# Optimization experiments

Measured on AMD Instinct MI355X. Metric: run time of the kernel, lower is better.

The kernel has to match this reference:

```python
import jax, jax.numpy as jnp
import numpy as np
from jax import lax

B, C, H, W = 8, 384, 32, 32
HEADS, GROUPS = 12, 3
CG = C // GROUPS          # 128 channels per offset group
HD = C // HEADS           # 32 head dim
NS = H * W                # sampled kv points (one per query location)
EPS = 1e-5


def setup_inputs() -> dict:
    key = jax.random.key(0)
    ks = jax.random.split(key, 10)
    w = lambda k, sh, sc=0.02: (jax.random.normal(k, sh, jnp.float32) * sc)
    return {
        "x1": jax.random.normal(ks[0], (B, C, H, W), jnp.float32),
        "x2": jax.random.normal(ks[1], (B, C, H, W), jnp.float32),
        "Wq": w(ks[2], (C, C)), "bq": jnp.zeros((C,), jnp.float32),
        "Wk": w(ks[3], (C, C)), "bk": jnp.zeros((C,), jnp.float32),
        "Wv": w(ks[4], (C, C)), "bv": jnp.zeros((C,), jnp.float32),
        "Wo": w(ks[5], (C, C)), "bo": jnp.zeros((C,), jnp.float32),
        "off_dw": w(ks[6], (CG, 1, 5, 5)),       # depthwise 5x5 offset conv
        "off_dw_b": jnp.zeros((CG,), jnp.float32),
        "ln_g": jnp.ones((CG,), jnp.float32),
        "ln_b": jnp.zeros((CG,), jnp.float32),
        "off_w": w(ks[7], (2, CG), 0.01),         # 1x1 conv -> 2 offset channels
    }


def _conv1x1(x, Wm, bm):
    return jnp.einsum('oc,bchw->bohw', Wm, x) + bm[None, :, None, None]


def _ref_grid():
    # normalized reference points in [-1,1], channel 0 = x (width), 1 = y (height)
    xs = (jnp.arange(W, dtype=jnp.float32) + 0.5) / W * 2.0 - 1.0
    ys = (jnp.arange(H, dtype=jnp.float32) + 0.5) / H * 2.0 - 1.0
    gy, gx = jnp.meshgrid(ys, xs, indexing='ij')   # [H,W]
    return jnp.stack([gx, gy], axis=0)             # [2,H,W]


def _forward(x1, x2, Wq, bq, Wk, bk, Wv, bv, Wo, bo,
             off_dw, off_dw_b, ln_g, ln_b, off_w):
    BG = B * GROUPS
    q = _conv1x1(x1, Wq, bq)                                   # [B,C,H,W]

    # --- offset network (per group) ---
    qg = q.reshape(BG, CG, H, W)
    t = lax.conv_general_dilated(qg, off_dw, (1, 1), 'SAME',
                                 dimension_numbers=('NCHW', 'OIHW', 'NCHW'),
                                 feature_group_count=CG)
    t = t + off_dw_b[None, :, None, None]
    mu = jnp.mean(t, axis=1, keepdims=True)
    var = jnp.var(t, axis=1, keepdims=True)
    t = (t - mu) * lax.rsqrt(var + EPS)
    t = t * ln_g[None, :, None, None] + ln_b[None, :, None, None]
    t = jax.nn.gelu(t)
    off = jnp.einsum('oc,bchw->bohw', off_w, t)                # [BG,2,H,W]

    pos = jnp.clip(off + _ref_grid()[None], -1.0, 1.0)         # [BG,2,H,W]
    px = pos[:, 0].reshape(BG, NS)
    py = pos[:, 1].reshape(BG, NS)

    # --- bilinear grid_sample of x2 (align_corners=True) ---
    ix = (px + 1.0) * 0.5 * (W - 1)
    iy = (py + 1.0) * 0.5 * (H - 1)
    x0f, y0f = jnp.floor(ix), jnp.floor(iy)
    wx, wy = ix - x0f, iy - y0f
    x0 = jnp.clip(x0f.astype(jnp.int32), 0, W - 1)
    x1i = jnp.clip(x0 + 1, 0, W - 1)
    y0 = jnp.clip(y0f.astype(jnp.int32), 0, H - 1)
    y1i = jnp.clip(y0 + 1, 0, H - 1)

    x2g = x2.reshape(BG, CG, H * W)

    def gather(yi, xi):
        idx = yi * W + xi                                      # [BG,NS]
        idx = jnp.broadcast_to(idx[:, None, :], (BG, CG, NS))
        return jnp.take_along_axis(x2g, idx, axis=2)           # [BG,CG,NS]

    v00, v01 = gather(y0, x0), gather(y0, x1i)
    v10, v11 = gather(y1i, x0), gather(y1i, x1i)
    wx_, wy_ = wx[:, None, :], wy[:, None, :]
    samp = (v00 * (1 - wx_) * (1 - wy_) + v01 * wx_ * (1 - wy_)
            + v10 * (1 - wx_) * wy_ + v11 * wx_ * wy_)         # [BG,CG,NS]
    samp = samp.reshape(B, C, NS)

    # --- multi-head attention between q and sampled k/v ---
    k = jnp.einsum('oc,bcn->bon', Wk, samp) + bk[None, :, None]
    v = jnp.einsum('oc,bcn->bon', Wv, samp) + bv[None, :, None]
    qf = q.reshape(B, HEADS, HD, NS)
    kf = k.reshape(B, HEADS, HD, NS)
    vf = v.reshape(B, HEADS, HD, NS)
    scale = 1.0 / np.sqrt(HD).astype(np.float32)
    attn = jax.nn.softmax(jnp.einsum('bhdq,bhdk->bhqk', qf * scale, kf), axis=-1)
    out = jnp.einsum('bhqk,bhdk->bhdq', attn, vf).reshape(B, C, H, W)
    y = _conv1x1(out, Wo, bo)
    return x1 + y                                              # residual add (drop_path=0 -> Identity)


def reference(x1, x2, Wq, bq, Wk, bk, Wv, bv, Wo, bo,
              off_dw, off_dw_b, ln_g, ln_b, off_w):
    return _forward(x1, x2, Wq, bq, Wk, bk, Wv, bv, Wo, bo,
                    off_dw, off_dw_b, ln_g, ln_b, off_w)
```

## Files before the change

### kernel.cpp

```cpp
#include <hip/hip_runtime.h>
#include <math.h>

#define B_  8
#define C_  384
#define NS_ 1024
#define HEADS_ 12
#define HD_ 32
#define GROUPS_ 3
#define CG_ 128
#define EPS_ 1e-5f
#define QSC2 (0.17677669529663687f * 1.4426950408889634f)

typedef __attribute__((ext_vector_type(8))) short bf16x8;
typedef __attribute__((ext_vector_type(4))) short bf16x4;
typedef __attribute__((ext_vector_type(4))) float f32x4;
typedef __attribute__((ext_vector_type(8))) __bf16 b8;

static __device__ __forceinline__ short f2b(float f) {
  union { float f; unsigned u; } v; v.f = f;
  unsigned r = v.u + 0x7fffu + ((v.u >> 16) & 1u);
  return (short)(r >> 16);
}
static __device__ __forceinline__ float b2f(short s) {
  union { unsigned u; float f; } v; v.u = ((unsigned)(unsigned short)s) << 16;
  return v.f;
}

#if __has_builtin(__builtin_amdgcn_exp2f)
#define EXP2(x) __builtin_amdgcn_exp2f(x)
#else
#define EXP2(x) exp2f(x)
#endif

static __device__ __forceinline__ unsigned cvtpk(float lo, float hi) {
  unsigned r;
  asm("v_cvt_pk_bf16_f32 %0, %1, %2" : "=v"(r) : "v"(lo), "v"(hi));
  return r;
}

static __device__ __forceinline__ f32x4 MFMA(bf16x8 a, bf16x8 b, f32x4 c) {
  return __builtin_amdgcn_mfma_f32_16x16x32_bf16(
      __builtin_bit_cast(b8, a), __builtin_bit_cast(b8, b), c, 0, 0, 0);
}

__global__ __launch_bounds__(256) void prep(
    const float* __restrict__ x1, const float* __restrict__ x2,
    const float* __restrict__ Wq, const float* __restrict__ Wk,
    const float* __restrict__ Wv, const float* __restrict__ Wo,
    const float* __restrict__ dw,
    short* __restrict__ x1t, short* __restrict__ x2t,
    short* __restrict__ Wqb, short* __restrict__ Wkb,
    short* __restrict__ Wvb, short* __restrict__ Wob,
    float* __restrict__ dwp) {
  __shared__ float tl[32][33];
  int id = blockIdx.x;
  int tid = threadIdx.x;
  int tx = tid & 31, ty = tid >> 5;
  if (id < 3072) {
    int nb = id & 31, cb = (id >> 5) % 12, b = id / 384;
    int n0 = nb * 32, c0 = cb * 32;
#pragma unroll
    for (int i = 0; i < 4; ++i)
      tl[ty + 8 * i][tx] = x1[((size_t)b * C_ + c0 + ty + 8 * i) * NS_ + n0 + tx];
    __syncthreads();
#pragma unroll
    for (int i = 0; i < 4; ++i)
      x1t[((size_t)b * NS_ + n0 + ty + 8 * i) * C_ + c0 + tx] = f2b(tl[tx][ty + 8 * i]);
  } else if (id < 6144) {
    int i = id - 3072;
    int nb = i & 31, cb = (i >> 5) & 3, bg = i / 128;
    int n0 = nb * 32, c0 = cb * 32;
#pragma unroll
    for (int j = 0; j < 4; ++j)
      tl[ty + 8 * j][tx] = x2[((size_t)bg * CG_ + c0 + ty + 8 * j) * NS_ + n0 + tx];
    __syncthreads();
#pragma unroll
    for (int j = 0; j < 4; ++j)
      x2t[((size_t)bg * NS_ + n0 + ty + 8 * j) * CG_ + c0 + tx] = f2b(tl[tx][ty + 8 * j]);
  } else if (id < 8448) {
    int i = id - 6144;
    int mat = i / 576;
    int e = (i % 576) * 256 + tid;
    const float* s = mat == 0 ? Wq : mat == 1 ? Wk : mat == 2 ? Wv : Wo;
    short*       d = mat == 0 ? Wqb : mat == 1 ? Wkb : mat == 2 ? Wvb : Wob;
    d[e] = f2b(s[e]);
  } else {
    int e = (id - 8448) * 256 + tid;
    if (e < 25 * CG_) { int t = e / CG_, c = e % CG_; dwp[e] = dw[c * 25 + t]; }
  }
}

#define GLOADA(kc_, AF)                                                        \
  _Pragma("unroll")                                                            \
  for (int rt = 0; rt < 4; ++rt)                                               \
    AF[rt] = *(const bf16x8*)(Ab + (size_t)(n0 + wr + rt * 16 + r15) * C_ +    \
                              (kc_) + g * 8);
#define GLOADB(kc_, BF, WP, MOFF)                                              \
  _Pragma("unroll")                                                            \
  for (int ct = 0; ct < 4; ++ct)                                               \
    BF[ct] = *(const bf16x8*)((WP) + (size_t)((MOFF) + ct * 16 + r15) * C_ +   \
                              (kc_) + g * 8);
#define GMFMA(AF, BF)                                                          \
  _Pragma("unroll")                                                            \
  for (int rt = 0; rt < 4; ++rt)                                               \
    _Pragma("unroll")                                                          \
    for (int ct = 0; ct < 4; ++ct) acc[rt][ct] = MFMA(AF[rt], BF[ct], acc[rt][ct]);

template <int MODE>
__global__ __launch_bounds__(256) void gemm_nm(
    const short* __restrict__ A, const short* __restrict__ Wb,
    const float* __restrict__ bias, const float* __restrict__ res,
    short* __restrict__ outb, float* __restrict__ outf) {
  int b = blockIdx.z;
  int n0 = blockIdx.x * 128;
  int m0 = blockIdx.y * 128;
  int wv = threadIdx.x >> 6;
  int lane = threadIdx.x & 63;
  int g = lane >> 4, r15 = lane & 15;
  int wr = (wv >> 1) * 64, wc = (wv & 1) * 64;

  const short* Ab = A + (size_t)b * NS_ * C_;
  f32x4 acc[4][4];
#pragma unroll
  for (int i = 0; i < 4; ++i)
#pragma unroll
    for (int j = 0; j < 4; ++j) acc[i][j] = (f32x4){0.f, 0.f, 0.f, 0.f};

  bf16x8 afA[4], bfA[4], afB[4], bfB[4];
  GLOADA(0, afA); GLOADB(0, bfA, Wb, m0 + wc);
#pragma unroll
  for (int cp = 0; cp < 6; ++cp) {
    GLOADA(64 * cp + 32, afB); GLOADB(64 * cp + 32, bfB, Wb, m0 + wc);
    GMFMA(afA, bfA);
    if (cp < 5) { GLOADA(64 * cp + 64, afA); GLOADB(64 * cp + 64, bfA, Wb, m0 + wc); }
    GMFMA(afB, bfB);
  }

#pragma unroll
  for (int rt = 0; rt < 4; ++rt)
#pragma unroll
    for (int ct = 0; ct < 4; ++ct) {
      int m = m0 + wc + ct * 16 + r15;
      int nb = n0 + wr + rt * 16 + g * 4;
      float bv = bias[m];
      f32x4 v = acc[rt][ct];
      v.x += bv; v.y += bv; v.z += bv; v.w += bv;
      if (MODE == 1) {
        *(f32x4*)(outf + ((size_t)b * C_ + m) * NS_ + nb) = v;
        outb[((size_t)b * NS_ + nb + 0) * C_ + m] = f2b(v.x * QSC2);
        outb[((size_t)b * NS_ + nb + 1) * C_ + m] = f2b(v.y * QSC2);
        outb[((size_t)b * NS_ + nb + 2) * C_ + m] = f2b(v.z * QSC2);
        outb[((size_t)b * NS_ + nb + 3) * C_ + m] = f2b(v.w * QSC2);
      } else {
        const f32x4 rv = *(const f32x4*)(res + ((size_t)b * C_ + m) * NS_ + nb);
        v.x += rv.x; v.y += rv.y; v.z += rv.z; v.w += rv.w;
        *(f32x4*)(outf + ((size_t)b * C_ + m) * NS_ + nb) = v;
      }
    }
}

__global__ __launch_bounds__(256) void gemm_kv(
    const short* __restrict__ A, const short* __restrict__ Wkb,
    const short* __restrict__ Wvb, const float* __restrict__ bkv,
    const float* __restrict__ bvv, short* __restrict__ kblk,
    short* __restrict__ vblk) {
  int b = blockIdx.z;
  int n0 = blockIdx.x * 128;
  int m0 = blockIdx.y * 64;
  int wv = threadIdx.x >> 6;
  int lane = threadIdx.x & 63;
  int g = lane >> 4, r15 = lane & 15;
  int wr = (wv >> 1) * 64;
  int isv = wv & 1;
  const short* Wsel = isv ? Wvb : Wkb;
  const float* bsel = isv ? bvv : bkv;

  const short* Ab = A + (size_t)b * NS_ * C_;
  f32x4 acc[4][4];
#pragma unroll
  for (int i = 0; i < 4; ++i)
#pragma unroll
    for (int j = 0; j < 4; ++j) acc[i][j] = (f32x4){0.f, 0.f, 0.f, 0.f};

  bf16x8 afA[4], bfA[4], afB[4], bfB[4];
  GLOADA(0, afA); GLOADB(0, bfA, Wsel, m0);
#pragma unroll
  for (int cp = 0; cp < 6; ++cp) {
    GLOADA(64 * cp + 32, afB); GLOADB(64 * cp + 32, bfB, Wsel, m0);
    GMFMA(afA, bfA);
    if (cp < 5) { GLOADA(64 * cp + 64, afA); GLOADB(64 * cp + 64, bfA, Wsel, m0); }
    GMFMA(afB, bfB);
  }

#pragma unroll
  for (int rt = 0; rt < 4; ++rt)
#pragma unroll
    for (int ct = 0; ct < 4; ++ct) {
      int m = m0 + ct * 16 + r15;
      int nb = n0 + wr + rt * 16 + g * 4;
      float bv = bsel[m];
      f32x4 v = acc[rt][ct];
      v.x += bv; v.y += bv; v.z += bv; v.w += bv;
      int h = m >> 5, dh = m & 31;
      if (!isv) {
        size_t hb = ((size_t)(b * HEADS_ + h) * 32 + (nb >> 5)) * 1024 +
                    (((nb >> 4) & 1) ? 512 : 0);
        int base_l = (nb & 15) | ((dh >> 3) << 4);
        int jj = dh & 7;
        kblk[hb + (size_t)(base_l + 0) * 8 + jj] = f2b(v.x);
        kblk[hb + (size_t)(base_l + 1) * 8 + jj] = f2b(v.y);
        kblk[hb + (size_t)(base_l + 2) * 8 + jj] = f2b(v.z);
        kblk[hb + (size_t)(base_l + 3) * 8 + jj] = f2b(v.w);
      } else {
        int dt = dh >> 4, q15v = dh & 15;
        int kk = nb & 31;
        int half = kk >> 4, gk = (kk & 15) >> 2;
        size_t off = ((size_t)(b * HEADS_ + h) * 32 + (nb >> 5)) * 1024 +
                     dt * 512 + (size_t)((q15v | (gk << 4))) * 8 + half * 4;
        bf16x4 s4 = {f2b(v.x), f2b(v.y), f2b(v.z), f2b(v.w)};
        *(bf16x4*)(vblk + off) = s4;
      }
    }
}

__global__ __launch_bounds__(256) void offsample4(
    const float* __restrict__ qd, const short* __restrict__ x2t,
    const float* __restrict__ dwp, const float* __restrict__ dwb,
    const float* __restrict__ lng, const float* __restrict__ lnb,
    const float* __restrict__ offw, short* __restrict__ samp) {
  int bg = blockIdx.x, y = blockIdx.y;
  int tid = threadIdx.x;
  int xg = tid >> 5, cc = tid & 31;
  int x0 = xg << 2, c0 = cc << 2;

  const float* qb = qd + ((size_t)bg * CG_ + c0) * NS_;

  f32x4 dwb4 = *(const f32x4*)(dwb + c0);
  float a[4][4];
#pragma unroll
  for (int i = 0; i < 4; ++i)
#pragma unroll
    for (int p = 0; p < 4; ++p) a[i][p] = dwb4[i];

#pragma unroll
  for (int dy = -2; dy <= 2; ++dy) {
    int yy = y + dy;
    if (yy < 0 || yy > 31) continue;
    f32x4 w0 = *(const f32x4*)(dwp + ((dy + 2) * 5 + 0) * CG_ + c0);
    f32x4 w1 = *(const f32x4*)(dwp + ((dy + 2) * 5 + 1) * CG_ + c0);
    f32x4 w2 = *(const f32x4*)(dwp + ((dy + 2) * 5 + 2) * CG_ + c0);
    f32x4 w3 = *(const f32x4*)(dwp + ((dy + 2) * 5 + 3) * CG_ + c0);
    f32x4 w4 = *(const f32x4*)(dwp + ((dy + 2) * 5 + 4) * CG_ + c0);
#pragma unroll
    for (int i = 0; i < 4; ++i) {
      const float* row = qb + (size_t)i * NS_ + yy * 32;
      f32x4 wa = (f32x4){0.f, 0.f, 0.f, 0.f};
      f32x4 wcv = (f32x4){0.f, 0.f, 0.f, 0.f};
      if (x0 >= 4)  wa  = *(const f32x4*)(row + x0 - 4);
      f32x4 wb = *(const f32x4*)(row + x0);
      if (x0 <= 24) wcv = *(const f32x4*)(row + x0 + 4);
      float w[12] = {wa[0], wa[1], wa[2], wa[3], wb[0], wb[1], wb[2], wb[3],
                     wcv[0], wcv[1], wcv[2], wcv[3]};
      float wt[5] = {w0[i], w1[i], w2[i], w3[i], w4[i]};
#pragma unroll
      for (int p = 0; p < 4; ++p)
#pragma unroll
        for (int j = 0; j < 5; ++j)
          a[i][p] = fmaf(w[p + j + 2], wt[j], a[i][p]);
    }
  }

  f32x4 sum = (f32x4){0.f, 0.f, 0.f, 0.f}, sumsq = sum;
#pragma unroll
  for (int i = 0; i < 4; ++i)
#pragma unroll
    for (int p = 0; p < 4; ++p) { sum[p] += a[i][p]; sumsq[p] += a[i][p] * a[i][p]; }
#pragma unroll
  for (int m = 1; m <= 16; m <<= 1) {
#pragma unroll
    for (int p = 0; p < 4; ++p) {
      sum[p]   += __shfl_xor(sum[p], m);
      sumsq[p] += __shfl_xor(sumsq[p], m);
    }
  }
  f32x4 mu, rs;
#pragma unroll
  for (int p = 0; p < 4; ++p) {
    mu[p] = sum[p] * (1.f / CG_);
    float var = sumsq[p] * (1.f / CG_) - mu[p] * mu[p];
    rs[p] = rsqrtf(var + EPS_);
  }

  f32x4 lg = *(const f32x4*)(lng + c0);
  f32x4 lb = *(const f32x4*)(lnb + c0);
  f32x4 ow0 = *(const f32x4*)(offw + c0);
  f32x4 ow1 = *(const f32x4*)(offw + CG_ + c0);
  f32x4 o0 = (f32x4){0.f, 0.f, 0.f, 0.f}, o1 = o0;
#pragma unroll
  for (int i = 0; i < 4; ++i)
#pragma unroll
    for (int p = 0; p < 4; ++p) {
      float z = (a[i][p] - mu[p]) * rs[p] * lg[i] + lb[i];
      float u = z * fmaf(0.044715f * z, z, 1.f);
      float e = __expf(-1.5957691216057308f * u);
      float ge = z * __builtin_amdgcn_rcpf(1.f + e);
      o0[p] = fmaf(ow0[i], ge, o0[p]);
      o1[p] = fmaf(ow1[i], ge, o1[p]);
    }
#pragma unroll
  for (int m = 1; m <= 16; m <<= 1) {
#pragma unroll
    for (int p = 0; p < 4; ++p) {
      o0[p] += __shfl_xor(o0[p], m);
      o1[p] += __shfl_xor(o1[p], m);
    }
  }

  int b = bg / GROUPS_, gi = bg % GROUPS_;
  const short* xb = x2t + (size_t)bg * NS_ * CG_ + c0;
  float gy = (y + 0.5f) * 0.0625f - 1.f;
#pragma unroll
  for (int p = 0; p < 4; ++p) {
    int x = x0 + p, n = y * 32 + x;
    float gx = (x + 0.5f) * 0.0625f - 1.f;
    float px = fminf(fmaxf(o0[p] + gx, -1.f), 1.f);
    float py = fminf(fmaxf(o1[p] + gy, -1.f), 1.f);
    float ix = (px + 1.f) * 0.5f * 31.f;
    float iy = (py + 1.f) * 0.5f * 31.f;
    float x0f = floorf(ix), y0f = floorf(iy);
    float wx = ix - x0f, wy = iy - y0f;
    int xa = min(max((int)x0f, 0), 31), xbb = min(xa + 1, 31);
    int ya = min(max((int)y0f, 0), 31), yb = min(ya + 1, 31);
    int i00 = ya * 32 + xa, i01 = ya * 32 + xbb;
    int i10 = yb * 32 + xa, i11 = yb * 32 + xbb;
    float w00 = (1.f - wx) * (1.f - wy), w01 = wx * (1.f - wy);
    float w10 = (1.f - wx) * wy,         w11 = wx * wy;
    bf16x4 v00 = *(const bf16x4*)(xb + (size_t)i00 * CG_);
    bf16x4 v01 = *(const bf16x4*)(xb + (size_t)i01 * CG_);
    bf16x4 v10 = *(const bf16x4*)(xb + (size_t)i10 * CG_);
    bf16x4 v11 = *(const bf16x4*)(xb + (size_t)i11 * CG_);
    short out4[4];
#pragma unroll
    for (int j = 0; j < 4; ++j) {
      float v = w00 * b2f(v00[j]) + w01 * b2f(v01[j]) +
                w10 * b2f(v10[j]) + w11 * b2f(v11[j]);
      out4[j] = f2b(v);
    }
    *(bf16x4*)(samp + ((size_t)b * NS_ + n) * C_ + gi * CG_ + c0) = *(bf16x4*)out4;
  }
}

__global__ __launch_bounds__(256) void attn_split(
    const short* __restrict__ qn, const short* __restrict__ kblk,
    const short* __restrict__ vblk, short* __restrict__ op0,
    short* __restrict__ op1, float* __restrict__ lp) {
  int L = blockIdx.x;
  int tq = L >> 3;
  int task = (L & 7) + ((tq % 24) << 3);
  int qblk = tq / 24;
  int bh = task >> 1, s = task & 1;
  int b = bh / HEADS_, h = bh % HEADS_;
  int wv = threadIdx.x >> 6, lane = threadIdx.x & 63;
  int g = lane >> 4, q15 = lane & 15;
  int q0 = qblk * 128 + wv * 32;

  const short* Qb = qn + (size_t)b * NS_ * C_ + h * HD_;
  const short* Kc = kblk + ((size_t)(b * HEADS_ + h) * 32 + s * 16) * 1024 + lane * 8;
  const short* Vc = vblk + ((size_t)(b * HEADS_ + h) * 32 + s * 16) * 1024 + lane * 8;

  bf16x8 qf[2];
  qf[0] = *(const bf16x8*)(Qb + (size_t)(q0 + q15) * C_ + g * 8);
  qf[1] = *(const bf16x8*)(Qb + (size_t)(q0 + 16 + q15) * C_ + g * 8);

  f32x4 o[2][2];
  o[0][0] = o[0][1] = o[1][0] = o[1][1] = (f32x4){0.f, 0.f, 0.f, 0.f};
  f32x4 lv[2];
  lv[0] = lv[1] = (f32x4){0.f, 0.f, 0.f, 0.f};

#define LOADC(c_, K0, K1, V0, V1)                                              \
  {                                                                            \
    K0 = *(const bf16x8*)(Kc + (c_) * 1024);                                   \
    K1 = *(const bf16x8*)(Kc + (c_) * 1024 + 512);                             \
    V0 = *(const bf16x8*)(Vc + (c_) * 1024);                                   \
    V1 = *(const bf16x8*)(Vc + (c_) * 1024 + 512);                             \
  }

#define COMPUTEC(K0, K1, V0, V1)                                               \
  {                                                                            \
    _Pragma("unroll")                                                          \
    for (int qt = 0; qt < 2; ++qt) {                                           \
      f32x4 z_ = {0.f, 0.f, 0.f, 0.f};                                         \
      f32x4 t0 = MFMA(K0, qf[qt], z_);                                         \
      f32x4 t1 = MFMA(K1, qf[qt], z_);                                         \
      f32x4 e0, e1;                                                            \
      e0.x = EXP2(t0.x); e0.y = EXP2(t0.y); e0.z = EXP2(t0.z); e0.w = EXP2(t0.w);\
      e1.x = EXP2(t1.x); e1.y = EXP2(t1.y); e1.z = EXP2(t1.z); e1.w = EXP2(t1.w);\
      lv[qt] += e0; lv[qt] += e1;                                              \
      union { unsigned u[4]; bf16x8 v; } pu;                                   \
      pu.u[0] = cvtpk(e0.x, e0.y);                                             \
      pu.u[1] = cvtpk(e0.z, e0.w);                                             \
      pu.u[2] = cvtpk(e1.x, e1.y);                                             \
      pu.u[3] = cvtpk(e1.z, e1.w);                                             \
      o[qt][0] = MFMA(V0, pu.v, o[qt][0]);                                     \
      o[qt][1] = MFMA(V1, pu.v, o[qt][1]);                                     \
    }                                                                          \
  }

  bf16x8 kA0, kA1, vA0, vA1, kB0, kB1, vB0, vB1;
  LOADC(0, kA0, kA1, vA0, vA1);
#pragma unroll
  for (int cp = 0; cp < 8; ++cp) {
    LOADC(2 * cp + 1, kB0, kB1, vB0, vB1);
    COMPUTEC(kA0, kA1, vA0, vA1);
    if (cp < 7) LOADC(2 * cp + 2, kA0, kA1, vA0, vA1);
    COMPUTEC(kB0, kB1, vB0, vB1);
  }
#undef LOADC
#undef COMPUTEC

  short* opS = s ? op1 : op0;
#pragma unroll
  for (int qt = 0; qt < 2; ++qt) {
    float lt = (lv[qt].x + lv[qt].y) + (lv[qt].z + lv[qt].w);
    lt += __shfl_xor(lt, 16);
    lt += __shfl_xor(lt, 32);
    int q = q0 + qt * 16 + q15;
    if (g == 0) lp[((size_t)(s * B_ + b) * HEADS_ + h) * NS_ + q] = lt;
#pragma unroll
    for (int dt = 0; dt < 2; ++dt) {
      f32x4 ov = o[qt][dt];
      bf16x4 s4 = {f2b(ov.x), f2b(ov.y), f2b(ov.z), f2b(ov.w)};
      *(bf16x4*)(opS + ((size_t)b * NS_ + q) * C_ + h * HD_ + dt * 16 + g * 4) = s4;
    }
  }
}

__global__ __launch_bounds__(256) void attn_merge(
    const short* __restrict__ op0, const short* __restrict__ op1,
    const float* __restrict__ lp, short* __restrict__ on) {
  int idx = blockIdx.x * 256 + threadIdx.x;
  int c8 = idx % (C_ / 8);
  int q  = (idx / (C_ / 8)) % NS_;
  int b  = idx / ((C_ / 8) * NS_);
  int c0 = c8 * 8, h = c0 >> 5;
  size_t off = ((size_t)b * NS_ + q) * C_ + c0;
  bf16x8 a  = *(const bf16x8*)(op0 + off);
  bf16x8 bb = *(const bf16x8*)(op1 + off);
  float l = lp[((size_t)b * HEADS_ + h) * NS_ + q] +
            lp[((size_t)(B_ + b) * HEADS_ + h) * NS_ + q];
  float rl = 1.f / l;
  short r[8];
#pragma unroll
  for (int j = 0; j < 8; ++j) r[j] = f2b((b2f(a[j]) + b2f(bb[j])) * rl);
  *(bf16x8*)(on + off) = *(bf16x8*)r;
}

extern "C" void kernel_launch(void* const* d_in, const int* in_sizes, int n_in,
                              void* d_out, int out_size, void* d_ws, size_t ws_size,
                              hipStream_t stream) {
  const float* x1      = (const float*)d_in[0];
  const float* x2      = (const float*)d_in[1];
  const float* Wq      = (const float*)d_in[2];
  const float* bq      = (const float*)d_in[3];
  const float* Wk      = (const float*)d_in[4];
  const float* bk      = (const float*)d_in[5];
  const float* Wv      = (const float*)d_in[6];
  const float* bv      = (const float*)d_in[7];
  const float* Wo      = (const float*)d_in[8];
  const float* bo      = (const float*)d_in[9];
  const float* off_dw  = (const float*)d_in[10];
  const float* off_dwb = (const float*)d_in[11];
  const float* ln_g    = (const float*)d_in[12];
  const float* ln_b    = (const float*)d_in[13];
  const float* off_w   = (const float*)d_in[14];

  char* base = (char*)d_ws;
  const size_t SZ = (size_t)B_ * C_ * NS_;
  float* q_dC  = (float*)base;
  short* q_nC  = (short*)(base + SZ * 4);
  short* samp  = (short*)(base + SZ * 6);
  short* k_blk = (short*)(base + SZ * 8);
  short* v_blk = (short*)(base + SZ * 10);
  short* o_nC  = (short*)(base + SZ * 12);
  short* x1t   = (short*)(base + SZ * 14);
  short* x2t   = (short*)(base + SZ * 16);
  short* Wqb   = (short*)(base + SZ * 18);
  short* Wkb   = Wqb + C_ * C_;
  short* Wvb   = Wkb + C_ * C_;
  short* Wob   = Wvb + C_ * C_;
  float* dwp   = (float*)(base + SZ * 18 + (size_t)8 * C_ * C_);
  short* op0   = samp;
  short* op1   = x1t;
  float* lp    = q_dC;

  dim3 gg(NS_ / 128, C_ / 128, B_);

  prep<<<dim3(8461), 256, 0, stream>>>(x1, x2, Wq, Wk, Wv, Wo, off_dw,
                                       x1t, x2t, Wqb, Wkb, Wvb, Wob, dwp);
  gemm_nm<1><<<gg, 256, 0, stream>>>(x1t, Wqb, bq, nullptr, q_nC, q_dC);
  offsample4<<<dim3(B_ * GROUPS_, 32), 256, 0, stream>>>(
      q_dC, x2t, dwp, off_dwb, ln_g, ln_b, off_w, samp);
  gemm_kv<<<dim3(NS_ / 128, C_ / 64, B_), 256, 0, stream>>>(
      samp, Wkb, Wvb, bk, bv, k_blk, v_blk);
  attn_split<<<dim3(1536), 256, 0, stream>>>(q_nC, k_blk, v_blk, op0, op1, lp);
  attn_merge<<<dim3(B_ * NS_ * (C_ / 8) / 256), 256, 0, stream>>>(op0, op1, lp, o_nC);
  gemm_nm<3><<<gg, 256, 0, stream>>>(o_nC, Wob, bo, x1, nullptr, (float*)d_out);
}
```

Measured before the change: 132.2 us.

## Fuse attention split-merge into output GEMM and double queries per attention wave

```diff
diff --git a/kernel.cpp b/kernel.cpp
--- a/kernel.cpp
+++ b/kernel.cpp
@@ -106,11 +106,10 @@
     _Pragma("unroll")                                                          \
     for (int ct = 0; ct < 4; ++ct) acc[rt][ct] = MFMA(AF[rt], BF[ct], acc[rt][ct]);
 
-template <int MODE>
-__global__ __launch_bounds__(256) void gemm_nm(
+__global__ __launch_bounds__(256) void gemm_q(
     const short* __restrict__ A, const short* __restrict__ Wb,
-    const float* __restrict__ bias, const float* __restrict__ res,
-    short* __restrict__ outb, float* __restrict__ outf) {
+    const float* __restrict__ bias, short* __restrict__ outb,
+    float* __restrict__ outf) {
   int b = blockIdx.z;
   int n0 = blockIdx.x * 128;
   int m0 = blockIdx.y * 128;
@@ -145,17 +144,73 @@
       float bv = bias[m];
       f32x4 v = acc[rt][ct];
       v.x += bv; v.y += bv; v.z += bv; v.w += bv;
-      if (MODE == 1) {
-        *(f32x4*)(outf + ((size_t)b * C_ + m) * NS_ + nb) = v;
-        outb[((size_t)b * NS_ + nb + 0) * C_ + m] = f2b(v.x * QSC2);
-        outb[((size_t)b * NS_ + nb + 1) * C_ + m] = f2b(v.y * QSC2);
-        outb[((size_t)b * NS_ + nb + 2) * C_ + m] = f2b(v.z * QSC2);
-        outb[((size_t)b * NS_ + nb + 3) * C_ + m] = f2b(v.w * QSC2);
-      } else {
-        const f32x4 rv = *(const f32x4*)(res + ((size_t)b * C_ + m) * NS_ + nb);
-        v.x += rv.x; v.y += rv.y; v.z += rv.z; v.w += rv.w;
-        *(f32x4*)(outf + ((size_t)b * C_ + m) * NS_ + nb) = v;
-      }
+      *(f32x4*)(outf + ((size_t)b * C_ + m) * NS_ + nb) = v;
+      outb[((size_t)b * NS_ + nb + 0) * C_ + m] = f2b(v.x * QSC2);
+      outb[((size_t)b * NS_ + nb + 1) * C_ + m] = f2b(v.y * QSC2);
+      outb[((size_t)b * NS_ + nb + 2) * C_ + m] = f2b(v.z * QSC2);
+      outb[((size_t)b * NS_ + nb + 3) * C_ + m] = f2b(v.w * QSC2);
+    }
+}
+
+#define GLOADAM(kc_, AF)                                                       \
+  _Pragma("unroll")                                                            \
+  for (int rt = 0; rt < 4; ++rt) {                                             \
+    int n_ = n0 + wr + rt * 16 + r15;                                          \
+    size_t off_ = ((size_t)bz * NS_ + n_) * C_ + (kc_) + g * 8;                \
+    bf16x8 a0_ = *(const bf16x8*)(op0 + off_);                                 \
+    bf16x8 a1_ = *(const bf16x8*)(op1 + off_);                                 \
+    int h_ = (kc_) >> 5;                                                       \
+    float l_ = lp[((size_t)(bz * HEADS_) + h_) * NS_ + n_] +                   \
+               lp[((size_t)((B_ + bz) * HEADS_) + h_) * NS_ + n_];             \
+    float rl_ = 1.f / l_;                                                      \
+    union { unsigned u[4]; bf16x8 v; } r_;                                     \
+    _Pragma("unroll")                                                          \
+    for (int j2 = 0; j2 < 4; ++j2)                                             \
+      r_.u[j2] = cvtpk((b2f(a0_[2 * j2]) + b2f(a1_[2 * j2])) * rl_,            \
+                       (b2f(a0_[2 * j2 + 1]) + b2f(a1_[2 * j2 + 1])) * rl_);   \
+    AF[rt] = r_.v;                                                             \
+  }
+
+__global__ __launch_bounds__(256) void gemm_of(
+    const short* __restrict__ op0, const short* __restrict__ op1,
+    const float* __restrict__ lp, const short* __restrict__ Wb,
+    const float* __restrict__ bias, const float* __restrict__ res,
+    float* __restrict__ outf) {
+  int bz = blockIdx.z;
+  int n0 = blockIdx.x * 128;
+  int m0 = blockIdx.y * 128;
+  int wv = threadIdx.x >> 6;
+  int lane = threadIdx.x & 63;
+  int g = lane >> 4, r15 = lane & 15;
+  int wr = (wv >> 1) * 64, wc = (wv & 1) * 64;
+
+  f32x4 acc[4][4];
+#pragma unroll
+  for (int i = 0; i < 4; ++i)
+#pragma unroll
+    for (int j = 0; j < 4; ++j) acc[i][j] = (f32x4){0.f, 0.f, 0.f, 0.f};
+
+  bf16x8 afA[4], bfA[4], afB[4], bfB[4];
+  GLOADAM(0, afA); GLOADB(0, bfA, Wb, m0 + wc);
+#pragma unroll
+  for (int cp = 0; cp < 6; ++cp) {
+    GLOADAM(64 * cp + 32, afB); GLOADB(64 * cp + 32, bfB, Wb, m0 + wc);
+    GMFMA(afA, bfA);
+    if (cp < 5) { GLOADAM(64 * cp + 64, afA); GLOADB(64 * cp + 64, bfA, Wb, m0 + wc); }
+    GMFMA(afB, bfB);
+  }
+
+#pragma unroll
+  for (int rt = 0; rt < 4; ++rt)
+#pragma unroll
+    for (int ct = 0; ct < 4; ++ct) {
+      int m = m0 + wc + ct * 16 + r15;
+      int nb = n0 + wr + rt * 16 + g * 4;
+      float bv = bias[m];
+      f32x4 v = acc[rt][ct];
+      const f32x4 rv = *(const f32x4*)(res + ((size_t)bz * C_ + m) * NS_ + nb);
+      v.x += bv + rv.x; v.y += bv + rv.y; v.z += bv + rv.z; v.w += bv + rv.w;
+      *(f32x4*)(outf + ((size_t)bz * C_ + m) * NS_ + nb) = v;
     }
 }
 
@@ -362,20 +417,21 @@
   int b = bh / HEADS_, h = bh % HEADS_;
   int wv = threadIdx.x >> 6, lane = threadIdx.x & 63;
   int g = lane >> 4, q15 = lane & 15;
-  int q0 = qblk * 128 + wv * 32;
+  int q0 = qblk * 256 + wv * 64;
 
   const short* Qb = qn + (size_t)b * NS_ * C_ + h * HD_;
   const short* Kc = kblk + ((size_t)(b * HEADS_ + h) * 32 + s * 16) * 1024 + lane * 8;
   const short* Vc = vblk + ((size_t)(b * HEADS_ + h) * 32 + s * 16) * 1024 + lane * 8;
 
-  bf16x8 qf[2];
-  qf[0] = *(const bf16x8*)(Qb + (size_t)(q0 + q15) * C_ + g * 8);
-  qf[1] = *(const bf16x8*)(Qb + (size_t)(q0 + 16 + q15) * C_ + g * 8);
-
-  f32x4 o[2][2];
-  o[0][0] = o[0][1] = o[1][0] = o[1][1] = (f32x4){0.f, 0.f, 0.f, 0.f};
-  f32x4 lv[2];
-  lv[0] = lv[1] = (f32x4){0.f, 0.f, 0.f, 0.f};
+  bf16x8 qf[4];
+#pragma unroll
+  for (int qt = 0; qt < 4; ++qt)
+    qf[qt] = *(const bf16x8*)(Qb + (size_t)(q0 + qt * 16 + q15) * C_ + g * 8);
+
+  f32x4 o[4][2];
+#pragma unroll
+  for (int qt = 0; qt < 4; ++qt) o[qt][0] = o[qt][1] = (f32x4){0.f, 0.f, 0.f, 0.f};
+  float l[4] = {0.f, 0.f, 0.f, 0.f};
 
 #define LOADC(c_, K0, K1, V0, V1)                                              \
   {                                                                            \
@@ -388,14 +444,14 @@
 #define COMPUTEC(K0, K1, V0, V1)                                               \
   {                                                                            \
     _Pragma("unroll")                                                          \
-    for (int qt = 0; qt < 2; ++qt) {                                           \
+    for (int qt = 0; qt < 4; ++qt) {                                           \
       f32x4 z_ = {0.f, 0.f, 0.f, 0.f};                                         \
       f32x4 t0 = MFMA(K0, qf[qt], z_);                                         \
       f32x4 t1 = MFMA(K1, qf[qt], z_);                                         \
       f32x4 e0, e1;                                                            \
       e0.x = EXP2(t0.x); e0.y = EXP2(t0.y); e0.z = EXP2(t0.z); e0.w = EXP2(t0.w);\
       e1.x = EXP2(t1.x); e1.y = EXP2(t1.y); e1.z = EXP2(t1.z); e1.w = EXP2(t1.w);\
-      lv[qt] += e0; lv[qt] += e1;                                              \
+      l[qt] += ((e0.x + e0.y) + (e0.z + e0.w)) + ((e1.x + e1.y) + (e1.z + e1.w));\
       union { unsigned u[4]; bf16x8 v; } pu;                                   \
       pu.u[0] = cvtpk(e0.x, e0.y);                                             \
       pu.u[1] = cvtpk(e0.z, e0.w);                                             \
@@ -420,8 +476,8 @@
 
   short* opS = s ? op1 : op0;
 #pragma unroll
-  for (int qt = 0; qt < 2; ++qt) {
-    float lt = (lv[qt].x + lv[qt].y) + (lv[qt].z + lv[qt].w);
+  for (int qt = 0; qt < 4; ++qt) {
+    float lt = l[qt];
     lt += __shfl_xor(lt, 16);
     lt += __shfl_xor(lt, 32);
     int q = q0 + qt * 16 + q15;
@@ -433,26 +489,6 @@
       *(bf16x4*)(opS + ((size_t)b * NS_ + q) * C_ + h * HD_ + dt * 16 + g * 4) = s4;
     }
   }
-}
-
-__global__ __launch_bounds__(256) void attn_merge(
-    const short* __restrict__ op0, const short* __restrict__ op1,
-    const float* __restrict__ lp, short* __restrict__ on) {
-  int idx = blockIdx.x * 256 + threadIdx.x;
-  int c8 = idx % (C_ / 8);
-  int q  = (idx / (C_ / 8)) % NS_;
-  int b  = idx / ((C_ / 8) * NS_);
-  int c0 = c8 * 8, h = c0 >> 5;
-  size_t off = ((size_t)b * NS_ + q) * C_ + c0;
-  bf16x8 a  = *(const bf16x8*)(op0 + off);
-  bf16x8 bb = *(const bf16x8*)(op1 + off);
-  float l = lp[((size_t)b * HEADS_ + h) * NS_ + q] +
-            lp[((size_t)(B_ + b) * HEADS_ + h) * NS_ + q];
-  float rl = 1.f / l;
-  short r[8];
-#pragma unroll
-  for (int j = 0; j < 8; ++j) r[j] = f2b((b2f(a[j]) + b2f(bb[j])) * rl);
-  *(bf16x8*)(on + off) = *(bf16x8*)r;
 }
 
 extern "C" void kernel_launch(void* const* d_in, const int* in_sizes, int n_in,
@@ -481,7 +517,6 @@
   short* samp  = (short*)(base + SZ * 6);
   short* k_blk = (short*)(base + SZ * 8);
   short* v_blk = (short*)(base + SZ * 10);
-  short* o_nC  = (short*)(base + SZ * 12);
   short* x1t   = (short*)(base + SZ * 14);
   short* x2t   = (short*)(base + SZ * 16);
   short* Wqb   = (short*)(base + SZ * 18);
@@ -497,12 +532,11 @@
 
   prep<<<dim3(8461), 256, 0, stream>>>(x1, x2, Wq, Wk, Wv, Wo, off_dw,
                                        x1t, x2t, Wqb, Wkb, Wvb, Wob, dwp);
-  gemm_nm<1><<<gg, 256, 0, stream>>>(x1t, Wqb, bq, nullptr, q_nC, q_dC);
+  gemm_q<<<gg, 256, 0, stream>>>(x1t, Wqb, bq, q_nC, q_dC);
   offsample4<<<dim3(B_ * GROUPS_, 32), 256, 0, stream>>>(
       q_dC, x2t, dwp, off_dwb, ln_g, ln_b, off_w, samp);
   gemm_kv<<<dim3(NS_ / 128, C_ / 64, B_), 256, 0, stream>>>(
       samp, Wkb, Wvb, bk, bv, k_blk, v_blk);
-  attn_split<<<dim3(1536), 256, 0, stream>>>(q_nC, k_blk, v_blk, op0, op1, lp);
-  attn_merge<<<dim3(B_ * NS_ * (C_ / 8) / 256), 256, 0, stream>>>(op0, op1, lp, o_nC);
-  gemm_nm<3><<<gg, 256, 0, stream>>>(o_nC, Wob, bo, x1, nullptr, (float*)d_out);
-}
+  attn_split<<<dim3(768), 256, 0, stream>>>(q_nC, k_blk, v_blk, op0, op1, lp);
+  gemm_of<<<gg, 256, 0, stream>>>(op0, op1, lp, Wob, bo, x1, (float*)d_out);
+}
```

After: 139.6 us. 1.06x slower.
